# Performance work log

Hardware: AMD Instinct MI355X
Metric: run time of the kernel (lower is better)

Reference implementation:

```python
import jax, jax.numpy as jnp
import numpy as np
import math

NH, DH, BS, LOCAL, RAND, NCLS = 12, 64, 49, 3, 3, 1
WINDOW = (8, 14, 14)
NKV = LOCAL + RAND


def make_rel_pos_index():
    ws = WINDOW
    rel_size = [2 * w - 1 for w in ws]
    coords = np.stack(np.meshgrid(*[np.arange(w) for w in ws], indexing='ij')).reshape(len(ws), -1)
    rel = (coords[:, :, None] - coords[:, None, :]).transpose(1, 2, 0).astype(np.int64)
    for i, w in enumerate(ws):
        rel[:, :, i] += w - 1
    for i, r in enumerate(rel_size[1:]):
        rel[:, :, :i + 1] *= r
    n = coords.shape[1]
    S = n + NCLS
    idx = np.zeros((S, S), dtype=np.int64)
    idx[NCLS:, NCLS:] = rel.sum(-1)
    start = int(np.prod(rel_size))
    idx[:NCLS, NCLS:] = np.arange(NCLS)[:, None] + start
    start += NCLS
    idx[NCLS:, :NCLS] = np.arange(NCLS)[None, :] + start
    start += NCLS
    idx[:NCLS, :NCLS] = np.arange(NCLS ** 2).reshape(NCLS, NCLS) + start
    return idx.astype(np.int32)


def setup_inputs() -> dict:
    key = jax.random.key(0)
    ks = jax.random.split(key, 8)
    B, S, D = 8, 1569, 768
    M = (S - NCLS) // BS  # 32 blocks
    hidden_states = jax.random.normal(ks[0], (B, S, D), dtype=jnp.float32)
    Wq = jax.random.normal(ks[1], (D, D), dtype=jnp.float32) * 0.02
    bq = jax.random.normal(ks[2], (D,), dtype=jnp.float32) * 0.02
    Wk = jax.random.normal(ks[3], (D, D), dtype=jnp.float32) * 0.02
    Wv = jax.random.normal(ks[4], (D, D), dtype=jnp.float32) * 0.02
    bv = jax.random.normal(ks[5], (D,), dtype=jnp.float32) * 0.02
    rel_table = jax.random.normal(ks[6], (10938, NH), dtype=jnp.float32) * 0.02
    rel_pos_index = jnp.asarray(make_rel_pos_index())
    rand_idx = jnp.sort(jax.random.randint(ks[7], (M, RAND), 0, M), axis=1).astype(jnp.int32)
    return {"hidden_states": hidden_states, "Wq": Wq, "bq": bq, "Wk": Wk, "Wv": Wv,
            "bv": bv, "rel_table": rel_table, "rel_pos_index": rel_pos_index, "rand_idx": rand_idx}


def reference(hidden_states, Wq, bq, Wk, Wv, bv, rel_table, rel_pos_index, rand_idx):
    B, S, D = hidden_states.shape
    scale = 1.0 / math.sqrt(DH)
    q = hidden_states @ Wq + bq
    k = hidden_states @ Wk          # key has no bias in BeitSelfAttention
    v = hidden_states @ Wv + bv
    split = lambda x: x.reshape(B, S, NH, DH).transpose(0, 2, 1, 3)  # b h s d
    q, k, v = split(q), split(k), split(v)

    # --- dense attention for cls queries over all keys ---
    cls_q = q[:, :, :NCLS]
    sim_cls = jnp.einsum('bhid,bhjd->bhij', cls_q, k) * scale
    bias_cls = rel_table[rel_pos_index[:NCLS, :]]           # [ncls, S, H]
    sim_cls = sim_cls + bias_cls.transpose(2, 0, 1)[None]
    attn_cls = jax.nn.softmax(sim_cls, axis=-1)
    out_cls = jnp.einsum('bhij,bhjd->bhid', attn_cls, v)    # [B,H,ncls,DH]

    # --- block-sparse attention for local queries ---
    loc_q = q[:, :, NCLS:]
    cls_k, loc_k = k[:, :, :NCLS], k[:, :, NCLS:]
    cls_v, loc_v = v[:, :, :NCLS], v[:, :, NCLS:]
    N = S - NCLS
    M = N // BS  # evenly divisible -> pad_q = 0
    qb = loc_q.reshape(B, NH, M, BS, DH)
    kb = loc_k.reshape(B, NH, M, BS, DH)
    vb = loc_v.reshape(B, NH, M, BS, DH)

    # local + random key-block indices per query block: [M, NKV]
    offs = jnp.arange(-(LOCAL // 2), LOCAL // 2 + 1)
    local_idx = (jnp.arange(M)[:, None] + offs[None, :]) % M
    attn_idx = jnp.concatenate([local_idx.astype(jnp.int32), rand_idx], axis=1)

    kg = kb[:, :, attn_idx]   # [B,H,M,NKV,BS,DH]
    vg = vb[:, :, attn_idx]

    sim_loc = jnp.einsum('bhmid,bhmnjd->bhminj', qb, kg).reshape(B, NH, M, BS, NKV * BS)
    sim_c = jnp.einsum('bhmid,bhjd->bhmij', qb, cls_k)       # [B,H,M,BS,ncls]
    sim = jnp.concatenate([sim_c, sim_loc], axis=-1) * scale

    # gathered relative-position bias: query tokens are ncls..S-1 in order
    key_tok = (NCLS + attn_idx[:, :, None] * BS + jnp.arange(BS)[None, None, :]).reshape(M, NKV * BS)
    to_idx = jnp.concatenate([jnp.broadcast_to(jnp.arange(NCLS)[None], (M, NCLS)), key_tok], axis=1)
    q_rows = rel_pos_index[NCLS:].reshape(M, BS, S)
    bias_idx = jnp.take_along_axis(q_rows, jnp.broadcast_to(to_idx[:, None, :], (M, BS, to_idx.shape[1])), axis=-1)
    bias = rel_table[bias_idx]                                # [M,BS,ncls+NKV*BS,H]
    sim = sim + bias.transpose(3, 0, 1, 2)[None]

    attn = jax.nn.softmax(sim, axis=-1)
    a_cls = attn[..., :NCLS]
    a_loc = attn[..., NCLS:].reshape(B, NH, M, BS, NKV, BS)
    out_loc = jnp.einsum('bhminj,bhmnjd->bhmid', a_loc, vg) \
            + jnp.einsum('bhmic,bhcd->bhmid', a_cls, cls_v)
    out_loc = out_loc.reshape(B, NH, N, DH)

    out = jnp.concatenate([out_cls, out_loc], axis=2)         # [B,H,S,DH]
    return out.transpose(0, 2, 1, 3).reshape(B, S, D)
```

## Files before the change

kernel.cpp:

```cpp
#include <hip/hip_runtime.h>


#define S_TOT   1569
#define NBATCH  8

__global__ __launch_bounds__(256) void gemm_f32(const float* __restrict__ hs,
                                                const float* __restrict__ Wq,
                                                const float* __restrict__ Wk,
                                                const float* __restrict__ Wv,
                                                const float* __restrict__ bq,
                                                const float* __restrict__ bv,
                                                float* __restrict__ Q,
                                                float* __restrict__ K,
                                                float* __restrict__ V,
                                                int b0, int nTok) {
    __shared__ float As[128][20];
    __shared__ float Bs[16][136];
    int tid = threadIdx.x;
    int t0 = blockIdx.x * 128;
    int n0 = blockIdx.y * 128;
    int which = n0 / 768;
    int ng0 = n0 - which * 768;
    const float* W = (which == 0) ? Wq : (which == 1 ? Wk : Wv);
    const float* Xb = hs + (size_t)b0 * S_TOT * 768;

    int tr = tid >> 4;
    int tc = tid & 15;

    int sat = tid >> 2;
    int sak = (tid & 3) * 4;
    int sbk = tid >> 4;
    int sbn = (tid & 15) * 8;

    float acc[8][8];
#pragma unroll
    for (int i = 0; i < 8; i++)
#pragma unroll
        for (int j = 0; j < 8; j++) acc[i][j] = 0.f;

    for (int k0 = 0; k0 < 768; k0 += 16) {
#pragma unroll
        for (int hh = 0; hh < 2; hh++) {
            int t = t0 + sat + hh * 64;
            float4 xv = make_float4(0.f, 0.f, 0.f, 0.f);
            if (t < nTok)
                xv = *(const float4*)(Xb + (size_t)t * 768 + k0 + sak);
            *(float4*)&As[sat + hh * 64][sak] = xv;
        }
        {
            const float* wr_ = W + (size_t)(k0 + sbk) * 768 + ng0 + sbn;
            *(float4*)&Bs[sbk][sbn]     = *(const float4*)(wr_);
            *(float4*)&Bs[sbk][sbn + 4] = *(const float4*)(wr_ + 4);
        }
        __syncthreads();

#pragma unroll
        for (int kq = 0; kq < 4; kq++) {
            float4 xa[8];
#pragma unroll
            for (int i = 0; i < 8; i++)
                xa[i] = *(const float4*)&As[tr * 8 + i][kq * 4];
#pragma unroll
            for (int kk = 0; kk < 4; kk++) {
                int k = kq * 4 + kk;
                float4 w0 = *(const float4*)&Bs[k][tc * 4];
                float4 w1 = *(const float4*)&Bs[k][64 + tc * 4];
#pragma unroll
                for (int i = 0; i < 8; i++) {
                    float a = (kk == 0) ? xa[i].x : (kk == 1) ? xa[i].y
                            : (kk == 2) ? xa[i].z : xa[i].w;
                    acc[i][0] = fmaf(a, w0.x, acc[i][0]);
                    acc[i][1] = fmaf(a, w0.y, acc[i][1]);
                    acc[i][2] = fmaf(a, w0.z, acc[i][2]);
                    acc[i][3] = fmaf(a, w0.w, acc[i][3]);
                    acc[i][4] = fmaf(a, w1.x, acc[i][4]);
                    acc[i][5] = fmaf(a, w1.y, acc[i][5]);
                    acc[i][6] = fmaf(a, w1.z, acc[i][6]);
                    acc[i][7] = fmaf(a, w1.w, acc[i][7]);
                }
            }
        }
        __syncthreads();
    }

    float* dst = (which == 0) ? Q : (which == 1 ? K : V);
    const float* bias = (which == 0) ? bq : (which == 2 ? bv : nullptr);
#pragma unroll
    for (int hh = 0; hh < 2; hh++) {
        int nn = ng0 + hh * 64 + tc * 4;
        int h = nn >> 6, d = nn & 63;
        float4 bv4 = make_float4(0.f, 0.f, 0.f, 0.f);
        if (bias) bv4 = *(const float4*)(bias + nn);
#pragma unroll
        for (int i = 0; i < 8; i++) {
            int t = t0 + tr * 8 + i;
            if (t >= nTok) continue;
            int bl = t / S_TOT;
            int s = t - bl * S_TOT;
            float4 o;
            o.x = acc[i][hh * 4 + 0] + bv4.x;
            o.y = acc[i][hh * 4 + 1] + bv4.y;
            o.z = acc[i][hh * 4 + 2] + bv4.z;
            o.w = acc[i][hh * 4 + 3] + bv4.w;
            *(float4*)(dst + ((size_t)(bl * 12 + h) * S_TOT + s) * 64 + d) = o;
        }
    }
}

__global__ __launch_bounds__(256) void cls_attn(const float* __restrict__ Q,
                                                const float* __restrict__ K,
                                                const float* __restrict__ V,
                                                const float* __restrict__ rel,
                                                const int* __restrict__ rpi,
                                                float* __restrict__ out, int b0) {
    int bh = blockIdx.x;
    int bl = bh / 12, h = bh - bl * 12;
    __shared__ float p[S_TOT];
    __shared__ float4 qs4[16];
    __shared__ float red[256];
    __shared__ float wred[8];
    int tid = threadIdx.x, lane = tid & 63, w = tid >> 6;
    size_t base = (size_t)bh * S_TOT * 64;
    const float* Qb = Q + base;
    const float* Kb = K + base;
    const float* Vb = V + base;
    if (tid < 64) ((float*)qs4)[tid] = Qb[tid];
    __syncthreads();

    float lmx = -1e30f;
    for (int j = tid; j < S_TOT; j += 256) {
        const float4* kr = (const float4*)(Kb + j * 64);
        float a = 0.f;
#pragma unroll
        for (int d4 = 0; d4 < 16; d4++) {
            float4 kv = kr[d4];
            float4 qv = qs4[d4];
            a = fmaf(qv.x, kv.x, a); a = fmaf(qv.y, kv.y, a);
            a = fmaf(qv.z, kv.z, a); a = fmaf(qv.w, kv.w, a);
        }
        a = a * 0.125f + rel[rpi[j] * 12 + h];
        p[j] = a;
        lmx = fmaxf(lmx, a);
    }
#pragma unroll
    for (int off = 32; off > 0; off >>= 1) lmx = fmaxf(lmx, __shfl_xor(lmx, off));
    if (lane == 0) wred[w] = lmx;
    __syncthreads();
    float mx = fmaxf(fmaxf(wred[0], wred[1]), fmaxf(wred[2], wred[3]));
    float lsum = 0.f;
    for (int j = tid; j < S_TOT; j += 256) {
        float e = __expf(p[j] - mx);
        p[j] = e;
        lsum += e;
    }
#pragma unroll
    for (int off = 32; off > 0; off >>= 1) lsum += __shfl_xor(lsum, off);
    if (lane == 0) wred[4 + w] = lsum;
    __syncthreads();
    float inv = 1.0f / (wred[4] + wred[5] + wred[6] + wred[7]);
    float acc = 0.f;
    for (int j = w; j < S_TOT; j += 4) acc = fmaf(p[j], Vb[j * 64 + lane], acc);
    red[w * 64 + lane] = acc;
    __syncthreads();
    if (w == 0) {
        float o = (red[lane] + red[64 + lane] + red[128 + lane] + red[192 + lane]) * inv;
        out[(size_t)(b0 + bl) * S_TOT * 768 + h * 64 + lane] = o;
    }
}

__global__ __launch_bounds__(256, 4) void loc_attn(const float* __restrict__ Q,
                                                   const float* __restrict__ K,
                                                   const float* __restrict__ V,
                                                   const float* __restrict__ rel,
                                                   const int* __restrict__ rand_idx,
                                                   float* __restrict__ out,
                                                   int b0, int ng) {
    int d = blockIdx.x;
    int xcd = d & 7, kk_ = d >> 3;
    int slot = xcd * (ng << 2) + kk_;
    int g = slot >> 5;
    int m = slot & 31;
    int h = g % 12;
    int bl = g / 12;

    __shared__ float Qlds[52][64];
    __shared__ float Plds[4][13][64];
    __shared__ int   tok[320];
    int tid = threadIdx.x, lane = tid & 63, w = tid >> 6;

    size_t base = (size_t)((bl * 12 + h) * S_TOT) * 64;
    const float* Qb = Q + base;
    const float* Kb = K + base;
    const float* Vb = V + base;

    for (int jj = tid; jj < 320; jj += 256) {
        int t = 0;
        if (jj >= 1 && jj < 295) {
            int j1 = jj - 1;
            int n = j1 / 49;
            int q = j1 - n * 49;
            int a;
            if (n == 0)      a = (m + 31) & 31;
            else if (n == 1) a = m;
            else if (n == 2) a = (m + 1) & 31;
            else             a = rand_idx[m * 3 + (n - 3)];
            t = 1 + a * 49 + q;
        }
        tok[jj] = t;
    }
    for (int idx = tid; idx < 52 * 64; idx += 256) {
        int r = idx >> 6, c = idx & 63;
        float qv = 0.f;
        if (r < 49) qv = Qb[(size_t)(1 + m * 49 + r) * 64 + c];
        ((float*)Qlds)[idx] = qv;
    }
    __syncthreads();

    int cq[13];
#pragma unroll
    for (int r = 0; r < 13; r++) {
        int i = w + 4 * r;
        int qr = 1 + m * 49 + i;
        if (qr > S_TOT - 1) qr = S_TOT - 1;
        int pq = qr - 1;
        int zq = pq / 196;
        int rem = pq - zq * 196;
        int yq = rem / 14;
        int xq = rem - yq * 14;
        cq[r] = zq * 729 + yq * 27 + xq;
    }

    float fm[13], fl[13], facc[13];
#pragma unroll
    for (int r = 0; r < 13; r++) { fm[r] = -1e30f; fl[r] = 0.f; facc[r] = 0.f; }

    for (int jc = 0; jc < 5; jc++) {
        int j = jc * 64 + lane;
        int tj = tok[j];
        const float* kp = Kb + (size_t)tj * 64;

        int pj = tj - 1;
        int zj = pj / 196;
        int remj = pj - zj * 196;
        int yj = remj / 14;
        int xj = remj - yj * 14;
        int cj = zj * 729 + yj * 27 + xj;
        bool iscls = (tj == 0);

        float s[13];
#pragma unroll
        for (int r = 0; r < 13; r++) s[r] = 0.f;
#pragma unroll 4
        for (int d4 = 0; d4 < 16; d4++) {
            float4 kv = *(const float4*)(kp + d4 * 4);
#pragma unroll
            for (int r = 0; r < 13; r++) {
                float4 qv = *(const float4*)&Qlds[w + 4 * r][d4 * 4];
                s[r] = fmaf(qv.x, kv.x, s[r]);
                s[r] = fmaf(qv.y, kv.y, s[r]);
                s[r] = fmaf(qv.z, kv.z, s[r]);
                s[r] = fmaf(qv.w, kv.w, s[r]);
            }
        }

        bool jv = j < 295;
#pragma unroll
        for (int r = 0; r < 13; r++) {
            int bidx = iscls ? 10936 : (cq[r] - cj + 5467);
            float sv = jv ? fmaf(s[r], 0.125f, rel[bidx * 12 + h])
                          : -1e30f;
            float mx = sv;
#pragma unroll
            for (int off = 32; off > 0; off >>= 1) mx = fmaxf(mx, __shfl_xor(mx, off));
            float mnew = fmaxf(fm[r], mx);
            float p = __expf(sv - mnew);
            float alpha = __expf(fm[r] - mnew);
            fm[r] = mnew;
            float ps = p;
#pragma unroll
            for (int off = 32; off > 0; off >>= 1) ps += __shfl_xor(ps, off);
            fl[r] = fmaf(fl[r], alpha, ps);
            facc[r] *= alpha;
            Plds[w][r][lane] = p;
        }

#pragma unroll 4
        for (int jg = 0; jg < 16; jg++) {
            int jb = jc * 64 + jg * 4;
            int t0 = tok[jb + 0], t1 = tok[jb + 1], t2 = tok[jb + 2], t3 = tok[jb + 3];
            float v0 = Vb[(size_t)t0 * 64 + lane];
            float v1 = Vb[(size_t)t1 * 64 + lane];
            float v2 = Vb[(size_t)t2 * 64 + lane];
            float v3 = Vb[(size_t)t3 * 64 + lane];
#pragma unroll
            for (int r = 0; r < 13; r++) {
                float4 p4 = *(const float4*)&Plds[w][r][jg * 4];
                facc[r] = fmaf(p4.x, v0, facc[r]);
                facc[r] = fmaf(p4.y, v1, facc[r]);
                facc[r] = fmaf(p4.z, v2, facc[r]);
                facc[r] = fmaf(p4.w, v3, facc[r]);
            }
        }
    }

    int nrows = (w == 0) ? 13 : 12;
    for (int r = 0; r < nrows; r++) {
        int i = w + 4 * r;
        int st = 1 + m * 49 + i;
        out[((size_t)(b0 + bl) * S_TOT + st) * 768 + h * 64 + lane] = facc[r] / fl[r];
    }
}

extern "C" void kernel_launch(void* const* d_in, const int* in_sizes, int n_in,
                              void* d_out, int out_size, void* d_ws, size_t ws_size,
                              hipStream_t stream) {
    (void)in_sizes; (void)n_in; (void)out_size;
    const float* hs  = (const float*)d_in[0];
    const float* Wq  = (const float*)d_in[1];
    const float* bq  = (const float*)d_in[2];
    const float* Wk  = (const float*)d_in[3];
    const float* Wv  = (const float*)d_in[4];
    const float* bv  = (const float*)d_in[5];
    const float* rel = (const float*)d_in[6];
    const int*   rpi = (const int*)d_in[7];
    const int*   rnd = (const int*)d_in[8];
    float* out = (float*)d_out;
    char* ws = (char*)d_ws;

    constexpr size_t PBUF = (size_t)12 * S_TOT * 64 * 4;

    int C = 1;
    if (ws_size >= 3 * PBUF) {
        size_t c = ws_size / (3 * PBUF);
        C = (c >= NBATCH) ? NBATCH : (int)c;
        if (C < 1) C = 1;
    }
    float* Q = (float*)(ws);
    float* K = (float*)(ws + (size_t)C * PBUF);
    float* V = (float*)(ws + (size_t)C * PBUF * 2);

    for (int b0 = 0; b0 < NBATCH; b0 += C) {
        int cb = (NBATCH - b0 < C) ? (NBATCH - b0) : C;
        int nTok = cb * S_TOT;
        gemm_f32<<<dim3((nTok + 127) / 128, 18), dim3(256), 0, stream>>>(
            hs, Wq, Wk, Wv, bq, bv, Q, K, V, b0, nTok);
        cls_attn<<<dim3(12 * cb), dim3(256), 0, stream>>>(Q, K, V, rel, rpi, out, b0);
        int ngrp = 12 * cb;
        loc_attn<<<dim3(32 * ngrp), dim3(256), 0, stream>>>(
            Q, K, V, rel, rnd, out, b0, ngrp);
    }
}
```

Measured before the change: 1.202 ms.

## Replace online softmax with single-pass exact softmax over all key chunks

Computes scores for all five 64-key chunks at once (65 accumulators per lane), then does a single max/exp/sum pass per row instead of an online-softmax rescale per chunk. This removes four rounds of shuffle reductions and alpha rescaling per row, and lets the five K loads per d4 step be issued together. The cost is much higher register pressure (s[5][13] plus the other per-lane arrays), which may cut occupancy or cause spills.

```diff
diff --git a/kernel.cpp b/kernel.cpp
--- a/kernel.cpp
+++ b/kernel.cpp
@@ -230,63 +230,95 @@
         cq[r] = zq * 729 + yq * 27 + xq;
     }
 
-    float fm[13], fl[13], facc[13];
-#pragma unroll
-    for (int r = 0; r < 13; r++) { fm[r] = -1e30f; fl[r] = 0.f; facc[r] = 0.f; }
-
-    for (int jc = 0; jc < 5; jc++) {
-        int j = jc * 64 + lane;
-        int tj = tok[j];
-        const float* kp = Kb + (size_t)tj * 64;
-
-        int pj = tj - 1;
+    const float* kp_[5];
+    int cj_[5];
+    bool cls_[5], jv_[5];
+#pragma unroll
+    for (int c = 0; c < 5; c++) {
+        int j = c * 64 + lane;
+        int t = tok[j];
+        kp_[c] = Kb + (size_t)t * 64;
+        int pj = t - 1;
         int zj = pj / 196;
         int remj = pj - zj * 196;
         int yj = remj / 14;
         int xj = remj - yj * 14;
-        int cj = zj * 729 + yj * 27 + xj;
-        bool iscls = (tj == 0);
-
-        float s[13];
-#pragma unroll
-        for (int r = 0; r < 13; r++) s[r] = 0.f;
+        cj_[c] = zj * 729 + yj * 27 + xj;
+        cls_[c] = (t == 0);
+        jv_[c] = (j < 295);
+    }
+
+    float s[5][13];
+#pragma unroll
+    for (int c = 0; c < 5; c++)
+#pragma unroll
+        for (int r = 0; r < 13; r++) s[c][r] = 0.f;
+
 #pragma unroll 4
-        for (int d4 = 0; d4 < 16; d4++) {
-            float4 kv = *(const float4*)(kp + d4 * 4);
-#pragma unroll
-            for (int r = 0; r < 13; r++) {
-                float4 qv = *(const float4*)&Qlds[w + 4 * r][d4 * 4];
-                s[r] = fmaf(qv.x, kv.x, s[r]);
-                s[r] = fmaf(qv.y, kv.y, s[r]);
-                s[r] = fmaf(qv.z, kv.z, s[r]);
-                s[r] = fmaf(qv.w, kv.w, s[r]);
-            }
-        }
-
-        bool jv = j < 295;
+    for (int d4 = 0; d4 < 16; d4++) {
+        float4 kv0 = *(const float4*)(kp_[0] + d4 * 4);
+        float4 kv1 = *(const float4*)(kp_[1] + d4 * 4);
+        float4 kv2 = *(const float4*)(kp_[2] + d4 * 4);
+        float4 kv3 = *(const float4*)(kp_[3] + d4 * 4);
+        float4 kv4 = *(const float4*)(kp_[4] + d4 * 4);
 #pragma unroll
         for (int r = 0; r < 13; r++) {
-            int bidx = iscls ? 10936 : (cq[r] - cj + 5467);
-            float sv = jv ? fmaf(s[r], 0.125f, rel[bidx * 12 + h])
-                          : -1e30f;
-            float mx = sv;
-#pragma unroll
-            for (int off = 32; off > 0; off >>= 1) mx = fmaxf(mx, __shfl_xor(mx, off));
-            float mnew = fmaxf(fm[r], mx);
-            float p = __expf(sv - mnew);
-            float alpha = __expf(fm[r] - mnew);
-            fm[r] = mnew;
-            float ps = p;
-#pragma unroll
-            for (int off = 32; off > 0; off >>= 1) ps += __shfl_xor(ps, off);
-            fl[r] = fmaf(fl[r], alpha, ps);
-            facc[r] *= alpha;
-            Plds[w][r][lane] = p;
-        }
-
+            float4 qv = *(const float4*)&Qlds[w + 4 * r][d4 * 4];
+            s[0][r] = fmaf(qv.x, kv0.x, s[0][r]); s[0][r] = fmaf(qv.y, kv0.y, s[0][r]);
+            s[0][r] = fmaf(qv.z, kv0.z, s[0][r]); s[0][r] = fmaf(qv.w, kv0.w, s[0][r]);
+            s[1][r] = fmaf(qv.x, kv1.x, s[1][r]); s[1][r] = fmaf(qv.y, kv1.y, s[1][r]);
+            s[1][r] = fmaf(qv.z, kv1.z, s[1][r]); s[1][r] = fmaf(qv.w, kv1.w, s[1][r]);
+            s[2][r] = fmaf(qv.x, kv2.x, s[2][r]); s[2][r] = fmaf(qv.y, kv2.y, s[2][r]);
+            s[2][r] = fmaf(qv.z, kv2.z, s[2][r]); s[2][r] = fmaf(qv.w, kv2.w, s[2][r]);
+            s[3][r] = fmaf(qv.x, kv3.x, s[3][r]); s[3][r] = fmaf(qv.y, kv3.y, s[3][r]);
+            s[3][r] = fmaf(qv.z, kv3.z, s[3][r]); s[3][r] = fmaf(qv.w, kv3.w, s[3][r]);
+            s[4][r] = fmaf(qv.x, kv4.x, s[4][r]); s[4][r] = fmaf(qv.y, kv4.y, s[4][r]);
+            s[4][r] = fmaf(qv.z, kv4.z, s[4][r]); s[4][r] = fmaf(qv.w, kv4.w, s[4][r]);
+        }
+    }
+
+    float fl[13];
+#pragma unroll
+    for (int r = 0; r < 13; r++) {
+        float sv0, sv1, sv2, sv3, sv4;
+        {
+            int b0i = cls_[0] ? 10936 : (cq[r] - cj_[0] + 5467);
+            int b1i = cls_[1] ? 10936 : (cq[r] - cj_[1] + 5467);
+            int b2i = cls_[2] ? 10936 : (cq[r] - cj_[2] + 5467);
+            int b3i = cls_[3] ? 10936 : (cq[r] - cj_[3] + 5467);
+            int b4i = cls_[4] ? 10936 : (cq[r] - cj_[4] + 5467);
+            sv0 = fmaf(s[0][r], 0.125f, rel[b0i * 12 + h]);
+            sv1 = fmaf(s[1][r], 0.125f, rel[b1i * 12 + h]);
+            sv2 = fmaf(s[2][r], 0.125f, rel[b2i * 12 + h]);
+            sv3 = fmaf(s[3][r], 0.125f, rel[b3i * 12 + h]);
+            sv4 = jv_[4] ? fmaf(s[4][r], 0.125f, rel[b4i * 12 + h]) : -1e30f;
+        }
+        float mx = fmaxf(fmaxf(fmaxf(sv0, sv1), fmaxf(sv2, sv3)), sv4);
+#pragma unroll
+        for (int off = 32; off > 0; off >>= 1) mx = fmaxf(mx, __shfl_xor(mx, off));
+        float e0 = __expf(sv0 - mx);
+        float e1 = __expf(sv1 - mx);
+        float e2 = __expf(sv2 - mx);
+        float e3 = __expf(sv3 - mx);
+        float e4 = __expf(sv4 - mx);
+        s[0][r] = e0; s[1][r] = e1; s[2][r] = e2; s[3][r] = e3; s[4][r] = e4;
+        float sum = ((e0 + e1) + (e2 + e3)) + e4;
+#pragma unroll
+        for (int off = 32; off > 0; off >>= 1) sum += __shfl_xor(sum, off);
+        fl[r] = sum;
+    }
+
+    float facc[13];
+#pragma unroll
+    for (int r = 0; r < 13; r++) facc[r] = 0.f;
+
+#pragma unroll
+    for (int c = 0; c < 5; c++) {
+#pragma unroll
+        for (int r = 0; r < 13; r++) Plds[w][r][lane] = s[c][r];
 #pragma unroll 4
         for (int jg = 0; jg < 16; jg++) {
-            int jb = jc * 64 + jg * 4;
+            int jb = c * 64 + jg * 4;
             int t0 = tok[jb + 0], t1 = tok[jb + 1], t2 = tok[jb + 2], t3 = tok[jb + 3];
             float v0 = Vb[(size_t)t0 * 64 + lane];
             float v1 = Vb[(size_t)t1 * 64 + lane];
```

Result: slower. 1.665 ms (+38.6%).
